# Kernel optimization log

Hardware: AMD Instinct MI355X
Metric: run time of the kernel (lower is better)

## Reference

```python
import jax, jax.numpy as jnp
import numpy as np
import math

C = 512

def setup_inputs() -> dict:
    key = jax.random.key(0)
    ks = jax.random.split(key, 9)
    s = 1.0 / math.sqrt(C)  # conv2d default init scale (uniform fan_in)
    x = jax.random.normal(ks[0], (4, C, 64, 64), dtype=jnp.float32)
    def w(k):
        return jax.random.uniform(k, (C, C), dtype=jnp.float32, minval=-s, maxval=s)
    def b(k):
        return jax.random.uniform(k, (C,), dtype=jnp.float32, minval=-s, maxval=s)
    return {
        'x': x,
        'wq': w(ks[1]), 'bq': b(ks[2]),
        'wk': w(ks[3]), 'bk': b(ks[4]),
        'wv': w(ks[5]), 'bv': b(ks[6]),
        'wp': w(ks[7]), 'bp': b(ks[8]),
    }

def _conv1x1(x, w, b):
    # x: [B,C,H,W]; 1x1 conv == channel-mixing matmul
    return jnp.einsum('oc,bchw->bohw', w, x) + b[None, :, None, None]

def reference(x, wq, bq, wk, bk, wv, bv, wp, bp):
    B, Cc, H, W = x.shape
    N = H * W
    q = _conv1x1(x, wq, bq).reshape(B, Cc, N)
    k = _conv1x1(x, wk, bk).reshape(B, Cc, N)
    v = _conv1x1(x, wv, bv).reshape(B, Cc, N)
    # attn[b,i,j] = sum_c q[b,c,i] k[b,c,j] / sqrt(C)
    attn = jnp.einsum('bci,bcj->bij', q, k) / math.sqrt(Cc)
    attn = jax.nn.softmax(attn, axis=-1)
    # out[b,c,i] = sum_j attn[b,i,j] v[b,c,j]
    out = jnp.einsum('bij,bcj->bci', attn, v).reshape(B, Cc, H, W)
    return x + _conv1x1(out, wp, bp)
```

## Files before the change

### kernel.cpp

```cpp
#include <hip/hip_runtime.h>
#include <hip/hip_bf16.h>
#include <stdint.h>

#define C_DIM 512
#define N_DIM 4096
#define B_DIM 4

typedef __bf16 bf16x8 __attribute__((ext_vector_type(8)));
typedef float f32x4 __attribute__((ext_vector_type(4)));
typedef int i32x8 __attribute__((ext_vector_type(8)));
#define AS1 __attribute__((address_space(1)))
#define AS3 __attribute__((address_space(3)))

static __device__ __forceinline__ unsigned short f2bf(float x) {
  unsigned u = __float_as_uint(x);
  unsigned r = (u + 0x7fffu + ((u >> 16) & 1u)) >> 16;
  return (unsigned short)r;
}
static __device__ __forceinline__ unsigned char f2fp8(float x) {
  return (unsigned char)__builtin_amdgcn_cvt_pk_fp8_f32(x, x, 0, false);
}

__global__ __launch_bounds__(256) void cvt_weights(
    const float* __restrict__ w0, const float* __restrict__ w1,
    const float* __restrict__ w2, const float* __restrict__ w3,
    unsigned short* __restrict__ o0, unsigned short* __restrict__ o1,
    unsigned short* __restrict__ o2, unsigned short* __restrict__ o3) {
  int i = blockIdx.x * blockDim.x + threadIdx.x;
  if (i < C_DIM * C_DIM) {
    o0[i] = f2bf(w0[i]); o1[i] = f2bf(w1[i]);
    o2[i] = f2bf(w2[i]); o3[i] = f2bf(w3[i]);
  }
}

__global__ __launch_bounds__(256) void transpose_x(
    const float* __restrict__ x, unsigned short* __restrict__ Xt) {
  __shared__ float t[32][33];
  const int b = blockIdx.z;
  const float* xb = x + (size_t)b * C_DIM * N_DIM;
  unsigned short* xtb = Xt + (size_t)b * N_DIM * C_DIM;
  const int n0 = blockIdx.x * 32, c0 = blockIdx.y * 32;
  const int tx = threadIdx.x, ty = threadIdx.y;
  #pragma unroll
  for (int i = ty; i < 32; i += 8)
    t[i][tx] = xb[(size_t)(c0 + i) * N_DIM + n0 + tx];
  __syncthreads();
  #pragma unroll
  for (int i = ty; i < 32; i += 8)
    xtb[(size_t)(n0 + i) * C_DIM + c0 + tx] = f2bf(t[tx][i]);
}

__global__ __launch_bounds__(256) void zero_buf(float* __restrict__ p, int n) {
  int i = blockIdx.x * 256 + threadIdx.x;
  if (i < n) p[i] = 0.f;
}

template<int BIAS, int OUT8>
__device__ __forceinline__ void gemm128_body(
    unsigned short* As, unsigned short* Bs,
    const unsigned short* __restrict__ A, const unsigned short* __restrict__ B,
    void* __restrict__ Cv, int K, int ldc,
    const float* __restrict__ bias, int bx, int by) {
  const int tid = threadIdx.x;
  const int wid = tid >> 6, lane = tid & 63;
  const int wm = (wid >> 1) * 64, wn = (wid & 1) * 64;
  f32x4 acc[4][4] = {};
  const size_t rowA0 = (size_t)bx * 128;
  const size_t rowB0 = (size_t)by * 128;
  const int sgrp = wid * 2;
  const int r0 = (sgrp * 64 + lane) >> 2;
  const int r1 = ((sgrp + 1) * 64 + lane) >> 2;
  const int cc = ((lane & 3) ^ ((lane >> 3) & 3)) * 8;
  const int lr = lane & 15;
  const int koff = (((lane >> 4) ^ ((lr >> 1) & 3))) * 8;

  for (int k0 = 0; k0 < K; k0 += 32) {
    __syncthreads();
    __builtin_amdgcn_global_load_lds(
        (const AS1 void*)(A + (rowA0 + r0) * K + k0 + cc),
        (AS3 void*)(As + sgrp * 512), 16, 0, 0);
    __builtin_amdgcn_global_load_lds(
        (const AS1 void*)(A + (rowA0 + r1) * K + k0 + cc),
        (AS3 void*)(As + (sgrp + 1) * 512), 16, 0, 0);
    __builtin_amdgcn_global_load_lds(
        (const AS1 void*)(B + (rowB0 + r0) * K + k0 + cc),
        (AS3 void*)(Bs + sgrp * 512), 16, 0, 0);
    __builtin_amdgcn_global_load_lds(
        (const AS1 void*)(B + (rowB0 + r1) * K + k0 + cc),
        (AS3 void*)(Bs + (sgrp + 1) * 512), 16, 0, 0);
    __syncthreads();
    bf16x8 af[4], bf[4];
    #pragma unroll
    for (int m = 0; m < 4; ++m)
      af[m] = *reinterpret_cast<const bf16x8*>(&As[(wm + m * 16 + lr) * 32 + koff]);
    #pragma unroll
    for (int n = 0; n < 4; ++n)
      bf[n] = *reinterpret_cast<const bf16x8*>(&Bs[(wn + n * 16 + lr) * 32 + koff]);
    #pragma unroll
    for (int m = 0; m < 4; ++m)
      #pragma unroll
      for (int n = 0; n < 4; ++n)
        acc[m][n] = __builtin_amdgcn_mfma_f32_16x16x32_bf16(af[m], bf[n], acc[m][n], 0, 0, 0);
  }

  const int rg = (lane >> 4) * 4;
  #pragma unroll
  for (int m = 0; m < 4; ++m) {
    #pragma unroll
    for (int n = 0; n < 4; ++n) {
      const int col = (int)rowB0 + wn + n * 16 + lr;
      #pragma unroll
      for (int r = 0; r < 4; ++r) {
        int row = (int)rowA0 + wm + m * 16 + rg + r;
        float v = acc[m][n][r];
        if (BIAS == 1) v += bias[col];
        if (OUT8)
          ((unsigned char*)Cv)[(size_t)row * ldc + col] = f2fp8(v);
        else
          ((unsigned short*)Cv)[(size_t)row * ldc + col] = f2bf(v);
      }
    }
  }
}

__global__ __launch_bounds__(256, 2) void gemm_qkv(
    const unsigned short* __restrict__ Xt,
    const unsigned short* __restrict__ Wq, const unsigned short* __restrict__ Wk,
    const unsigned short* __restrict__ Wv,
    const float* __restrict__ bq, const float* __restrict__ bk,
    const float* __restrict__ bv,
    unsigned char* __restrict__ Qb, unsigned char* __restrict__ Kb,
    unsigned short* __restrict__ Vb) {
  __shared__ unsigned short As[4096], Bs[4096];
  const long NCe = (long)N_DIM * C_DIM;
  const int z = blockIdx.z;
  const int wsel = z % 3, bat = z / 3;
  const unsigned short* Xz = Xt + (size_t)bat * NCe;
  if (wsel == 0) {
    gemm128_body<1, 1>(As, Bs, Xz, Wq, Qb + (size_t)bat * NCe, C_DIM, C_DIM,
                       bq, blockIdx.x, blockIdx.y);
  } else if (wsel == 1) {
    gemm128_body<1, 1>(As, Bs, Xz, Wk, Kb + (size_t)bat * NCe, C_DIM, C_DIM,
                       bk, blockIdx.x, blockIdx.y);
  } else {
    gemm128_body<1, 0>(As, Bs, Xz, Wv, Vb + (size_t)bat * NCe, C_DIM, C_DIM,
                       bv, blockIdx.x, blockIdx.y);
  }
}

__global__ __launch_bounds__(256, 2) void gemm_pvt(
    const unsigned short* __restrict__ Wp, const unsigned short* __restrict__ Vb,
    unsigned char* __restrict__ PVt) {
  __shared__ unsigned short As[4096], Bs[4096];
  const long NCe = (long)N_DIM * C_DIM;
  const long PVe = (long)C_DIM * N_DIM;
  const int z = blockIdx.z;
  gemm128_body<0, 1>(As, Bs, Wp, Vb + (size_t)z * NCe, PVt + (size_t)z * PVe,
                     C_DIM, N_DIM, nullptr, blockIdx.x, blockIdx.y);
}

template<int MFR, int MODE, int GX, int GY>
__global__ __launch_bounds__(256, 3) void gemm_mx(
    const unsigned char* __restrict__ A, long sA,
    const unsigned char* __restrict__ B, long sB,
    void* __restrict__ Cp, long sC,
    int K, int lda, int ldb, int ldc, float scale,
    const float* __restrict__ bias,
    float* __restrict__ denom, long sDen,
    const float* __restrict__ resid, long sR) {
  constexpr int MT = MFR * 32;
  constexpr int WM = MFR * 16;
  __shared__ unsigned char Asm[MT * 128], Bsm[16384];

  int flat = blockIdx.x + GX * (blockIdx.y + GY * blockIdx.z);
  const int nwg = GX * GY * gridDim.z;
  flat = (flat & 7) * (nwg >> 3) + (flat >> 3);
  const int bx = flat & (GX - 1);
  const int by = (flat / GX) & (GY - 1);
  const int z  = flat / (GX * GY);

  const unsigned char* Ag = A + (size_t)z * sA + (size_t)bx * MT * lda;
  const unsigned char* Bg = B + (size_t)z * sB + (size_t)by * 128 * ldb;
  const int tid = threadIdx.x;
  const int wid = tid >> 6, lane = tid & 63;
  const int wm = (wid >> 1) * WM, wn = (wid & 1) * 64;
  const int lr = lane & 15, q = lane >> 4;
  const int g16 = ((lane & 7) ^ ((lane >> 3) & 7)) * 16;
  const int rl = lr & 7;
  const int rb0 = (((2 * q) ^ rl)) * 16;
  const int rb1 = (((2 * q + 1) ^ rl)) * 16;

  f32x4 acc[MFR][4] = {};
  const int NT = K >> 7;

  for (int t = 0; t < NT; ++t) {
    __syncthreads();
    const int k0 = t << 7;
    #pragma unroll
    for (int i = 0; i < MFR; ++i) {
      const int rr = (i * 4 + wid) * 8 + (lane >> 3);
      __builtin_amdgcn_global_load_lds(
          (const AS1 void*)(Ag + (size_t)rr * lda + k0 + g16),
          (AS3 void*)(Asm + (i * 4 + wid) * 1024), 16, 0, 0);
    }
    #pragma unroll
    for (int i = 0; i < 4; ++i) {
      const int rr = (i * 4 + wid) * 8 + (lane >> 3);
      __builtin_amdgcn_global_load_lds(
          (const AS1 void*)(Bg + (size_t)rr * ldb + k0 + g16),
          (AS3 void*)(Bsm + (i * 4 + wid) * 1024), 16, 0, 0);
    }
    __syncthreads();

    i32x8 bf[4], af[MFR];
    #pragma unroll
    for (int n = 0; n < 4; ++n) {
      const unsigned char* rp = Bsm + (wn + n * 16 + lr) * 128;
      *reinterpret_cast<uint4*>(&bf[n]) = *reinterpret_cast<const uint4*>(rp + rb0);
      *(reinterpret_cast<uint4*>(&bf[n]) + 1) = *reinterpret_cast<const uint4*>(rp + rb1);
    }
    #pragma unroll
    for (int mi = 0; mi < MFR; ++mi) {
      const unsigned char* rp = Asm + (wm + mi * 16 + lr) * 128;
      *reinterpret_cast<uint4*>(&af[mi]) = *reinterpret_cast<const uint4*>(rp + rb0);
      *(reinterpret_cast<uint4*>(&af[mi]) + 1) = *reinterpret_cast<const uint4*>(rp + rb1);
    }
    __builtin_amdgcn_s_setprio(1);
    #pragma unroll
    for (int mi = 0; mi < MFR; ++mi)
      #pragma unroll
      for (int n = 0; n < 4; ++n)
        acc[mi][n] = __builtin_amdgcn_mfma_scale_f32_16x16x128_f8f6f4(
            af[mi], bf[n], acc[mi][n], 0, 0, 0, 127, 0, 127);
    __builtin_amdgcn_s_setprio(0);
  }

  const int rg = q * 4;
  if (MODE == 0) {
    unsigned char* Co = (unsigned char*)Cp + (size_t)z * sC;
    float* Dz = denom + (size_t)z * sDen;
    #pragma unroll
    for (int m = 0; m < MFR; ++m) {
      float ev[4][4];
      #pragma unroll
      for (int n = 0; n < 4; ++n) {
        const int col = by * 128 + wn + n * 16 + lr;
        #pragma unroll
        for (int r = 0; r < 4; ++r) {
          int row = bx * MT + wm + m * 16 + rg + r;
          ev[n][r] = __expf(acc[m][n][r] * scale);
          Co[(size_t)row * ldc + col] = f2fp8(ev[n][r]);
        }
      }
      #pragma unroll
      for (int r = 0; r < 4; ++r) {
        float s = (ev[0][r] + ev[1][r]) + (ev[2][r] + ev[3][r]);
        s += __shfl_xor(s, 1); s += __shfl_xor(s, 2);
        s += __shfl_xor(s, 4); s += __shfl_xor(s, 8);
        if (lr == 0) {
          int row = bx * MT + wm + m * 16 + rg + r;
          atomicAdd(&Dz[row], s);
        }
      }
    }
  } else {
    float* Co = (float*)Cp + (size_t)z * sC;
    const float* Rs = resid + (size_t)z * sR;
    const float* Dz = denom + (size_t)z * sDen;
    #pragma unroll
    for (int n = 0; n < 4; ++n) {
      const int col = by * 128 + wn + n * 16 + lr;
      const float dinv = 1.0f / Dz[col];
      #pragma unroll
      for (int m = 0; m < MFR; ++m)
        #pragma unroll
        for (int r = 0; r < 4; ++r) {
          int row = bx * MT + wm + m * 16 + rg + r;
          size_t idx = (size_t)row * ldc + col;
          Co[idx] = acc[m][n][r] * dinv + bias[row] + Rs[idx];
        }
    }
  }
}

extern "C" void kernel_launch(void* const* d_in, const int* in_sizes, int n_in,
                              void* d_out, int out_size, void* d_ws, size_t ws_size,
                              hipStream_t stream) {
  const float* x  = (const float*)d_in[0];
  const float* wq = (const float*)d_in[1];
  const float* bq = (const float*)d_in[2];
  const float* wk = (const float*)d_in[3];
  const float* bk = (const float*)d_in[4];
  const float* wv = (const float*)d_in[5];
  const float* bv = (const float*)d_in[6];
  const float* wp = (const float*)d_in[7];
  const float* bp = (const float*)d_in[8];
  float* out = (float*)d_out;
  char* ws = (char*)d_ws;
  const size_t MB = 1024 * 1024;
  unsigned short* Wq  = (unsigned short*)(ws + 0);
  unsigned short* Wk  = (unsigned short*)(ws + 512 * 1024);
  unsigned short* Wv  = (unsigned short*)(ws + 1 * MB);
  unsigned short* Wp  = (unsigned short*)(ws + MB + 512 * 1024);
  unsigned short* Xt  = (unsigned short*)(ws + 2 * MB);
  unsigned char*  Qb8 = (unsigned char*)(ws + 18 * MB);
  unsigned char*  Kb8 = (unsigned char*)(ws + 26 * MB);
  unsigned short* Vb  = (unsigned short*)(ws + 34 * MB);
  unsigned char*  PVt = (unsigned char*)(ws + 50 * MB);
  float* denom = (float*)(ws + 58 * MB);
  unsigned char*  P8  = (unsigned char*)(ws + 59 * MB);
  const long NCe = (long)N_DIM * C_DIM;
  const long NNe = (long)N_DIM * N_DIM;
  const long PVe = (long)C_DIM * N_DIM;
  const float rs = 0.044194173824159216f;
  const bool big = ws_size >= 59 * MB + 4 * (size_t)N_DIM * N_DIM;

  cvt_weights<<<dim3((C_DIM * C_DIM + 255) / 256), 256, 0, stream>>>(
      wq, wk, wv, wp, Wq, Wk, Wv, Wp);
  transpose_x<<<dim3(N_DIM / 32, C_DIM / 32, B_DIM), dim3(32, 8), 0, stream>>>(x, Xt);
  gemm_qkv<<<dim3(32, 4, 12), 256, 0, stream>>>(
      Xt, Wq, Wk, Wv, bq, bk, bv, Qb8, Kb8, Vb);
  gemm_pvt<<<dim3(4, 32, 4), 256, 0, stream>>>(Wp, Vb, PVt);
  zero_buf<<<dim3(B_DIM * N_DIM / 256), 256, 0, stream>>>(denom, B_DIM * N_DIM);

  if (big) {
    gemm_mx<4, 0, 32, 32><<<dim3(32, 32, 4), 256, 0, stream>>>(
        Qb8, NCe, Kb8, NCe, P8, NNe, C_DIM, C_DIM, C_DIM, N_DIM, rs,
        nullptr, denom, N_DIM, nullptr, 0);
    gemm_mx<2, 1, 8, 32><<<dim3(8, 32, 4), 256, 0, stream>>>(
        PVt, PVe, P8, NNe, out, NCe, N_DIM, N_DIM, N_DIM, N_DIM, 1.0f,
        bp, denom, N_DIM, x, NCe);
  } else {
    for (int b = 0; b < B_DIM; ++b) {
      gemm_mx<4, 0, 32, 32><<<dim3(32, 32, 1), 256, 0, stream>>>(
          Qb8 + (size_t)b * NCe, 0, Kb8 + (size_t)b * NCe, 0, P8, 0,
          C_DIM, C_DIM, C_DIM, N_DIM, rs, nullptr, denom + (size_t)b * N_DIM, 0,
          nullptr, 0);
      gemm_mx<2, 1, 8, 32><<<dim3(8, 32, 1), 256, 0, stream>>>(
          PVt + (size_t)b * PVe, 0, P8, 0, (void*)(out + (size_t)b * NCe), 0,
          N_DIM, N_DIM, N_DIM, N_DIM, 1.0f, bp, denom + (size_t)b * N_DIM, 0,
          x + (size_t)b * NCe, 0);
    }
  }
}
```

Measured before the change: 188.4 us.

## Fold output projection into V weights and double-buffer fp8 attention GEMMs

Precomputes Wp·Wv and Wp·bv once, so the per-batch PV^T projection comes straight from X in the same launch as Q and K. This removes the separate V GEMM, the bf16 V buffer and the second per-batch projection GEMM. The fp8 attention GEMM main loop also gets double-buffered LDS, with explicit vmcnt waits and barriers so the next tile's global-to-LDS loads overlap the current tile's MFMAs. The cost is more LDS per block, which may lower occupancy, plus small extra kernels for the weight product and bias vector.

```diff
diff --git a/kernel.cpp b/kernel.cpp
--- a/kernel.cpp
+++ b/kernel.cpp
@@ -21,16 +21,39 @@
   return (unsigned char)__builtin_amdgcn_cvt_pk_fp8_f32(x, x, 0, false);
 }
 
-__global__ __launch_bounds__(256) void cvt_weights(
-    const float* __restrict__ w0, const float* __restrict__ w1,
-    const float* __restrict__ w2, const float* __restrict__ w3,
-    unsigned short* __restrict__ o0, unsigned short* __restrict__ o1,
-    unsigned short* __restrict__ o2, unsigned short* __restrict__ o3) {
-  int i = blockIdx.x * blockDim.x + threadIdx.x;
-  if (i < C_DIM * C_DIM) {
-    o0[i] = f2bf(w0[i]); o1[i] = f2bf(w1[i]);
-    o2[i] = f2bf(w2[i]); o3[i] = f2bf(w3[i]);
-  }
+__global__ __launch_bounds__(256) void cvtT_weights(
+    const float* __restrict__ wq, const float* __restrict__ wk,
+    const float* __restrict__ wv, const float* __restrict__ wp,
+    unsigned short* __restrict__ oq, unsigned short* __restrict__ ok,
+    unsigned short* __restrict__ ovt, unsigned short* __restrict__ op) {
+  __shared__ float t[32][33];
+  const int zz = blockIdx.z;
+  const float* w = zz == 0 ? wq : zz == 1 ? wk : zz == 2 ? wv : wp;
+  unsigned short* o = zz == 0 ? oq : zz == 1 ? ok : zz == 2 ? ovt : op;
+  const int r0 = blockIdx.y * 32, c0 = blockIdx.x * 32;
+  const int tx = threadIdx.x, ty = threadIdx.y;
+  if (zz == 2) {
+    #pragma unroll
+    for (int i = ty; i < 32; i += 8) t[i][tx] = w[(r0 + i) * C_DIM + c0 + tx];
+    __syncthreads();
+    #pragma unroll
+    for (int i = ty; i < 32; i += 8)
+      o[(size_t)(c0 + i) * C_DIM + r0 + tx] = f2bf(t[tx][i]);
+  } else {
+    #pragma unroll
+    for (int i = ty; i < 32; i += 8)
+      o[(size_t)(r0 + i) * C_DIM + c0 + tx] = f2bf(w[(r0 + i) * C_DIM + c0 + tx]);
+  }
+}
+
+__global__ __launch_bounds__(512) void vec_bvp(
+    const float* __restrict__ wp, const float* __restrict__ bv,
+    float* __restrict__ bvp) {
+  const int t = threadIdx.x;
+  float s = 0.f;
+  #pragma unroll 8
+  for (int m = 0; m < C_DIM; ++m) s += wp[(size_t)t * C_DIM + m] * bv[m];
+  bvp[t] = s;
 }
 
 __global__ __launch_bounds__(256) void transpose_x(
@@ -114,6 +137,7 @@
         int row = (int)rowA0 + wm + m * 16 + rg + r;
         float v = acc[m][n][r];
         if (BIAS == 1) v += bias[col];
+        if (BIAS == 2) v += bias[row];
         if (OUT8)
           ((unsigned char*)Cv)[(size_t)row * ldc + col] = f2fp8(v);
         else
@@ -123,41 +147,41 @@
   }
 }
 
-__global__ __launch_bounds__(256, 2) void gemm_qkv(
+__global__ __launch_bounds__(256, 2) void gemm_wpv(
+    const unsigned short* __restrict__ Wp, const unsigned short* __restrict__ Wvt,
+    unsigned short* __restrict__ Wpv) {
+  __shared__ unsigned short As[4096], Bs[4096];
+  gemm128_body<0, 0>(As, Bs, Wp, Wvt, Wpv, C_DIM, C_DIM, nullptr,
+                     blockIdx.x, blockIdx.y);
+}
+
+__global__ __launch_bounds__(256, 2) void gemm_proj(
     const unsigned short* __restrict__ Xt,
     const unsigned short* __restrict__ Wq, const unsigned short* __restrict__ Wk,
-    const unsigned short* __restrict__ Wv,
+    const unsigned short* __restrict__ Wpv,
     const float* __restrict__ bq, const float* __restrict__ bk,
-    const float* __restrict__ bv,
+    const float* __restrict__ bvp,
     unsigned char* __restrict__ Qb, unsigned char* __restrict__ Kb,
-    unsigned short* __restrict__ Vb) {
-  __shared__ unsigned short As[4096], Bs[4096];
-  const long NCe = (long)N_DIM * C_DIM;
-  const int z = blockIdx.z;
-  const int wsel = z % 3, bat = z / 3;
-  const unsigned short* Xz = Xt + (size_t)bat * NCe;
-  if (wsel == 0) {
-    gemm128_body<1, 1>(As, Bs, Xz, Wq, Qb + (size_t)bat * NCe, C_DIM, C_DIM,
-                       bq, blockIdx.x, blockIdx.y);
-  } else if (wsel == 1) {
-    gemm128_body<1, 1>(As, Bs, Xz, Wk, Kb + (size_t)bat * NCe, C_DIM, C_DIM,
-                       bk, blockIdx.x, blockIdx.y);
-  } else {
-    gemm128_body<1, 0>(As, Bs, Xz, Wv, Vb + (size_t)bat * NCe, C_DIM, C_DIM,
-                       bv, blockIdx.x, blockIdx.y);
-  }
-}
-
-__global__ __launch_bounds__(256, 2) void gemm_pvt(
-    const unsigned short* __restrict__ Wp, const unsigned short* __restrict__ Vb,
     unsigned char* __restrict__ PVt) {
   __shared__ unsigned short As[4096], Bs[4096];
   const long NCe = (long)N_DIM * C_DIM;
   const long PVe = (long)C_DIM * N_DIM;
-  const int z = blockIdx.z;
-  gemm128_body<0, 1>(As, Bs, Wp, Vb + (size_t)z * NCe, PVt + (size_t)z * PVe,
-                     C_DIM, N_DIM, nullptr, blockIdx.x, blockIdx.y);
-}
+  const int sel = blockIdx.z >> 2, bat = blockIdx.z & 3;
+  const unsigned short* Xz = Xt + (size_t)bat * NCe;
+  if (sel == 0) {
+    gemm128_body<1, 1>(As, Bs, Xz, Wq, Qb + (size_t)bat * NCe, C_DIM, C_DIM,
+                       bq, blockIdx.x, blockIdx.y);
+  } else if (sel == 1) {
+    gemm128_body<1, 1>(As, Bs, Xz, Wk, Kb + (size_t)bat * NCe, C_DIM, C_DIM,
+                       bk, blockIdx.x, blockIdx.y);
+  } else {
+    gemm128_body<2, 1>(As, Bs, Wpv, Xz, PVt + (size_t)bat * PVe, C_DIM, N_DIM,
+                       bvp, blockIdx.y, blockIdx.x);
+  }
+}
+
+#define BAR() do { asm volatile("" ::: "memory"); __builtin_amdgcn_s_barrier(); \
+                   asm volatile("" ::: "memory"); } while (0)
 
 template<int MFR, int MODE, int GX, int GY>
 __global__ __launch_bounds__(256, 3) void gemm_mx(
@@ -168,9 +192,10 @@
     const float* __restrict__ bias,
     float* __restrict__ denom, long sDen,
     const float* __restrict__ resid, long sR) {
-  constexpr int MT = MFR * 32;
-  constexpr int WM = MFR * 16;
-  __shared__ unsigned char Asm[MT * 128], Bsm[16384];
+  constexpr int MT   = MFR * 32;
+  constexpr int WM   = MFR * 16;
+  constexpr int ABUF = MT * 128;
+  __shared__ unsigned char Asm[2 * ABUF], Bsm[2 * 16384];
 
   int flat = blockIdx.x + GX * (blockIdx.y + GY * blockIdx.z);
   const int nwg = GX * GY * gridDim.z;
@@ -190,38 +215,37 @@
   const int rb0 = (((2 * q) ^ rl)) * 16;
   const int rb1 = (((2 * q + 1) ^ rl)) * 16;
 
-  f32x4 acc[MFR][4] = {};
-  const int NT = K >> 7;
-
-  for (int t = 0; t < NT; ++t) {
-    __syncthreads();
-    const int k0 = t << 7;
+  auto STAGE = [&](int P, int tt) {
+    const int k0 = tt << 7;
     #pragma unroll
     for (int i = 0; i < MFR; ++i) {
       const int rr = (i * 4 + wid) * 8 + (lane >> 3);
       __builtin_amdgcn_global_load_lds(
           (const AS1 void*)(Ag + (size_t)rr * lda + k0 + g16),
-          (AS3 void*)(Asm + (i * 4 + wid) * 1024), 16, 0, 0);
+          (AS3 void*)(Asm + P * ABUF + (i * 4 + wid) * 1024), 16, 0, 0);
     }
     #pragma unroll
     for (int i = 0; i < 4; ++i) {
       const int rr = (i * 4 + wid) * 8 + (lane >> 3);
       __builtin_amdgcn_global_load_lds(
           (const AS1 void*)(Bg + (size_t)rr * ldb + k0 + g16),
-          (AS3 void*)(Bsm + (i * 4 + wid) * 1024), 16, 0, 0);
-    }
-    __syncthreads();
-
+          (AS3 void*)(Bsm + P * 16384 + (i * 4 + wid) * 1024), 16, 0, 0);
+    }
+  };
+
+  f32x4 acc[MFR][4] = {};
+
+  auto BODY = [&](int P) {
     i32x8 bf[4], af[MFR];
     #pragma unroll
     for (int n = 0; n < 4; ++n) {
-      const unsigned char* rp = Bsm + (wn + n * 16 + lr) * 128;
+      const unsigned char* rp = Bsm + P * 16384 + (wn + n * 16 + lr) * 128;
       *reinterpret_cast<uint4*>(&bf[n]) = *reinterpret_cast<const uint4*>(rp + rb0);
       *(reinterpret_cast<uint4*>(&bf[n]) + 1) = *reinterpret_cast<const uint4*>(rp + rb1);
     }
     #pragma unroll
     for (int mi = 0; mi < MFR; ++mi) {
-      const unsigned char* rp = Asm + (wm + mi * 16 + lr) * 128;
+      const unsigned char* rp = Asm + P * ABUF + (wm + mi * 16 + lr) * 128;
       *reinterpret_cast<uint4*>(&af[mi]) = *reinterpret_cast<const uint4*>(rp + rb0);
       *(reinterpret_cast<uint4*>(&af[mi]) + 1) = *reinterpret_cast<const uint4*>(rp + rb1);
     }
@@ -233,6 +257,31 @@
         acc[mi][n] = __builtin_amdgcn_mfma_scale_f32_16x16x128_f8f6f4(
             af[mi], bf[n], acc[mi][n], 0, 0, 0, 127, 0, 127);
     __builtin_amdgcn_s_setprio(0);
+  };
+
+  auto WAITV = [&]() {
+    if (MFR == 4) asm volatile("s_waitcnt vmcnt(8)" ::: "memory");
+    else          asm volatile("s_waitcnt vmcnt(6)" ::: "memory");
+  };
+
+  const int NT = K >> 7;
+  STAGE(0, 0); STAGE(1, 1);
+  WAITV();
+  BAR();
+
+  for (int t = 0; t < NT; t += 2) {
+    BODY(0);
+    BAR();
+    if (t + 2 < NT) { STAGE(0, t + 2); WAITV(); }
+    else { asm volatile("s_waitcnt vmcnt(0)" ::: "memory"); }
+    BAR();
+    BODY(1);
+    if (t + 2 < NT) {
+      BAR();
+      if (t + 3 < NT) { STAGE(1, t + 3); WAITV(); }
+      else { asm volatile("s_waitcnt vmcnt(0)" ::: "memory"); }
+      BAR();
+    }
   }
 
   const int rg = q * 4;
@@ -300,27 +349,29 @@
   const size_t MB = 1024 * 1024;
   unsigned short* Wq  = (unsigned short*)(ws + 0);
   unsigned short* Wk  = (unsigned short*)(ws + 512 * 1024);
-  unsigned short* Wv  = (unsigned short*)(ws + 1 * MB);
+  unsigned short* Wvt = (unsigned short*)(ws + 1 * MB);
   unsigned short* Wp  = (unsigned short*)(ws + MB + 512 * 1024);
-  unsigned short* Xt  = (unsigned short*)(ws + 2 * MB);
-  unsigned char*  Qb8 = (unsigned char*)(ws + 18 * MB);
-  unsigned char*  Kb8 = (unsigned char*)(ws + 26 * MB);
-  unsigned short* Vb  = (unsigned short*)(ws + 34 * MB);
-  unsigned char*  PVt = (unsigned char*)(ws + 50 * MB);
-  float* denom = (float*)(ws + 58 * MB);
-  unsigned char*  P8  = (unsigned char*)(ws + 59 * MB);
+  unsigned short* Wpv = (unsigned short*)(ws + 2 * MB);
+  float* bvp = (float*)(ws + 2 * MB + 512 * 1024);
+  unsigned short* Xt  = (unsigned short*)(ws + 3 * MB);
+  unsigned char*  Qb8 = (unsigned char*)(ws + 19 * MB);
+  unsigned char*  Kb8 = (unsigned char*)(ws + 27 * MB);
+  unsigned char*  PVt = (unsigned char*)(ws + 35 * MB);
+  float* denom = (float*)(ws + 43 * MB);
+  unsigned char*  P8  = (unsigned char*)(ws + 44 * MB);
   const long NCe = (long)N_DIM * C_DIM;
   const long NNe = (long)N_DIM * N_DIM;
   const long PVe = (long)C_DIM * N_DIM;
   const float rs = 0.044194173824159216f;
-  const bool big = ws_size >= 59 * MB + 4 * (size_t)N_DIM * N_DIM;
-
-  cvt_weights<<<dim3((C_DIM * C_DIM + 255) / 256), 256, 0, stream>>>(
-      wq, wk, wv, wp, Wq, Wk, Wv, Wp);
+  const bool big = ws_size >= 44 * MB + 4 * (size_t)N_DIM * N_DIM;
+
+  cvtT_weights<<<dim3(16, 16, 4), dim3(32, 8), 0, stream>>>(
+      wq, wk, wv, wp, Wq, Wk, Wvt, Wp);
+  vec_bvp<<<dim3(1), dim3(512), 0, stream>>>(wp, bv, bvp);
+  gemm_wpv<<<dim3(4, 4, 1), 256, 0, stream>>>(Wp, Wvt, Wpv);
   transpose_x<<<dim3(N_DIM / 32, C_DIM / 32, B_DIM), dim3(32, 8), 0, stream>>>(x, Xt);
-  gemm_qkv<<<dim3(32, 4, 12), 256, 0, stream>>>(
-      Xt, Wq, Wk, Wv, bq, bk, bv, Qb8, Kb8, Vb);
-  gemm_pvt<<<dim3(4, 32, 4), 256, 0, stream>>>(Wp, Vb, PVt);
+  gemm_proj<<<dim3(32, 4, 12), 256, 0, stream>>>(
+      Xt, Wq, Wk, Wpv, bq, bk, bvp, Qb8, Kb8, PVt);
   zero_buf<<<dim3(B_DIM * N_DIM / 256), 256, 0, stream>>>(denom, B_DIM * N_DIM);
 
   if (big) {
```

After: 276.7 us. 46.8% more time.
